# Kernel optimization log

Measured on AMD Instinct MI355X. Metric: run time of the kernel, lower is better.

Reference implementation:

```python
import jax, jax.numpy as jnp
import numpy as np

EPS_LN = 1e-5


def segment_softmax(logits, seg, num_segments):
    m = jax.ops.segment_max(logits, seg, num_segments=num_segments)
    e = jnp.exp(logits - m[seg])
    s = jax.ops.segment_sum(e, seg, num_segments=num_segments)
    return e / (s[seg] + 1e-16)


def transformer_conv(x, src, dst, edge_attr, Wq, bq, Wk, bk, Wv, bv, We, Ws, bs):
    # PyG TransformerConv, heads=1: key/value gathered at source, query at dst,
    # transformed edge feature added to both key and value (message).
    N, D = x.shape[0], Wq.shape[1]
    q = (x @ Wq + bq)[dst]                      # [E, D]
    e = edge_attr @ We                          # [E, D] (lin_edge, no bias)
    k = (x @ Wk + bk)[src] + e                  # [E, D]
    v = (x @ Wv + bv)[src] + e                  # [E, D]
    alpha = segment_softmax((q * k).sum(-1) / jnp.sqrt(jnp.float32(D)), dst, N)
    agg = jax.ops.segment_sum(alpha[:, None] * v, dst, num_segments=N)
    return agg + x @ Ws + bs                    # root_weight skip connection


def graph_layer_norm(x, w, b):
    # PyG LayerNorm mode='graph': normalize over all nodes AND features of the graph.
    mu = x.mean()
    xc = x - mu
    var = (xc * xc).mean()
    return xc * jax.lax.rsqrt(var + EPS_LN) * w + b


def setup_inputs():
    key = jax.random.key(0)
    ks = jax.random.split(key, 32)
    N, E, F_NODE, F_EDGE, H, D_OUT = 50000, 800000, 64, 16, 128, 1
    g = lambda k, shp, s=0.05: jax.random.normal(k, shp, jnp.float32) * s
    inp = {
        'x': jax.random.normal(ks[0], (N, F_NODE), jnp.float32),
        'edge_index': jax.random.randint(ks[1], (2, E), 0, N),
        'edge_attr': jax.random.normal(ks[2], (E, F_EDGE), jnp.float32),
        'fc1_w': g(ks[3], (F_NODE, H)), 'fc1_b': jnp.zeros((H,), jnp.float32),
        'c1_Wq': g(ks[4], (H, H)), 'c1_bq': jnp.zeros((H,), jnp.float32),
        'c1_Wk': g(ks[5], (H, H)), 'c1_bk': jnp.zeros((H,), jnp.float32),
        'c1_Wv': g(ks[6], (H, H)), 'c1_bv': jnp.zeros((H,), jnp.float32),
        'c1_We': g(ks[7], (F_EDGE, H)),
        'c1_Ws': g(ks[8], (H, H)), 'c1_bs': jnp.zeros((H,), jnp.float32),
        'ln1_w': jnp.ones((H,), jnp.float32), 'ln1_b': jnp.zeros((H,), jnp.float32),
        'c2_Wq': g(ks[9], (H, H)), 'c2_bq': jnp.zeros((H,), jnp.float32),
        'c2_Wk': g(ks[10], (H, H)), 'c2_bk': jnp.zeros((H,), jnp.float32),
        'c2_Wv': g(ks[11], (H, H)), 'c2_bv': jnp.zeros((H,), jnp.float32),
        'c2_We': g(ks[12], (F_EDGE, H)),
        'c2_Ws': g(ks[13], (H, H)), 'c2_bs': jnp.zeros((H,), jnp.float32),
        'ln2_w': jnp.ones((H,), jnp.float32), 'ln2_b': jnp.zeros((H,), jnp.float32),
        'fc2_w': g(ks[14], (H, D_OUT)), 'fc2_b': jnp.zeros((D_OUT,), jnp.float32),
    }
    return inp


def reference(x, edge_index, edge_attr,
              fc1_w, fc1_b,
              c1_Wq, c1_bq, c1_Wk, c1_bk, c1_Wv, c1_bv, c1_We, c1_Ws, c1_bs,
              ln1_w, ln1_b,
              c2_Wq, c2_bq, c2_Wk, c2_bk, c2_Wv, c2_bv, c2_We, c2_Ws, c2_bs,
              ln2_w, ln2_b,
              fc2_w, fc2_b):
    src, dst = edge_index[0], edge_index[1]
    hx = x @ fc1_w + fc1_b
    h = transformer_conv(hx, src, dst, edge_attr,
                         c1_Wq, c1_bq, c1_Wk, c1_bk, c1_Wv, c1_bv, c1_We, c1_Ws, c1_bs)
    h = jax.nn.relu(graph_layer_norm(h, ln1_w, ln1_b))
    h = transformer_conv(h, src, dst, edge_attr,
                         c2_Wq, c2_bq, c2_Wk, c2_bk, c2_Wv, c2_bv, c2_We, c2_Ws, c2_bs)
    h = jax.nn.relu(graph_layer_norm(h, ln2_w, ln2_b))
    return h @ fc2_w + fc2_b
```

## Files before the change

### kernel.cpp

```cpp
#include <hip/hip_runtime.h>
#include <math.h>

#define HH 128
#define FIN 64
#define FE 16
#define SCAN_CHUNK 512

__global__ __launch_bounds__(256) void zero_int4(int4* __restrict__ p, int n4) {
  const int stride = gridDim.x * 256;
  for (int i = blockIdx.x * 256 + threadIdx.x; i < n4; i += stride)
    p[i] = make_int4(0, 0, 0, 0);
}

__global__ __launch_bounds__(256) void hist_kernel(
    const int* __restrict__ dstArr, int* __restrict__ deg, int E) {
  const int e = blockIdx.x * 256 + threadIdx.x;
  if (e < E) atomicAdd(deg + dstArr[e], 1);
}

__global__ __launch_bounds__(256) void scan1(
    const int* __restrict__ deg, int* __restrict__ out, int* __restrict__ sums, int n) {
  __shared__ int lds[256];
  const int t = threadIdx.x;
  const int i0 = blockIdx.x * SCAN_CHUNK + t * 2;
  const int v0 = (i0 < n) ? deg[i0] : 0;
  const int v1 = (i0 + 1 < n) ? deg[i0 + 1] : 0;
  const int tsum = v0 + v1;
  lds[t] = tsum;
  __syncthreads();
  for (int off = 1; off < 256; off <<= 1) {
    const int x = (t >= off) ? lds[t - off] : 0;
    __syncthreads();
    lds[t] += x;
    __syncthreads();
  }
  const int excl = lds[t] - tsum;
  if (i0 < n) out[i0] = excl;
  if (i0 + 1 < n) out[i0 + 1] = excl + v0;
  if (t == 255) sums[blockIdx.x] = lds[255];
}

__global__ __launch_bounds__(256) void scan2(int* __restrict__ sums, int nb) {
  __shared__ int lds[256];
  const int t = threadIdx.x;
  const int v = (t < nb) ? sums[t] : 0;
  lds[t] = v;
  __syncthreads();
  for (int off = 1; off < 256; off <<= 1) {
    const int x = (t >= off) ? lds[t - off] : 0;
    __syncthreads();
    lds[t] += x;
    __syncthreads();
  }
  if (t < nb) sums[t] = lds[t] - v;
}

__global__ __launch_bounds__(256) void scan3(
    int* __restrict__ out, const int* __restrict__ sums, int n) {
  const int add = sums[blockIdx.x];
  const int i0 = blockIdx.x * SCAN_CHUNK + threadIdx.x * 2;
  if (i0 < n) out[i0] += add;
  if (i0 + 1 < n) out[i0 + 1] += add;
}

__global__ __launch_bounds__(256) void scatter_kernel(
    const int* __restrict__ dstArr, const int* __restrict__ off,
    int* __restrict__ cursor, int* __restrict__ eids, int E) {
  const int e = blockIdx.x * 256 + threadIdx.x;
  if (e < E) {
    const int d = dstArr[e];
    const int p = atomicAdd(cursor + d, 1);
    eids[off[d] + p] = e;
  }
}

template<int K, int RB>
__global__ __launch_bounds__(128) void gemm_rows(
    const float* __restrict__ in, const float* __restrict__ W,
    const float* __restrict__ bias, float* __restrict__ out, int nrows) {
  __shared__ float tile[RB * K];
  const int r0 = blockIdx.x * RB;
  const int tid = threadIdx.x;
  {
    const int rows = min(RB, nrows - r0);
    const int cnt = rows * K / 4;
    const float4* src = (const float4*)(in + (size_t)r0 * K);
    float4* dst = (float4*)tile;
    for (int i = tid; i < cnt; i += 128) dst[i] = src[i];
  }
  __syncthreads();
  const int j = tid;
  float acc[RB];
  const float bj = bias[j];
#pragma unroll
  for (int r = 0; r < RB; ++r) acc[r] = bj;
#pragma unroll 4
  for (int k = 0; k < K; ++k) {
    float w = W[k * HH + j];
#pragma unroll
    for (int r = 0; r < RB; ++r) acc[r] += tile[r * K + k] * w;
  }
#pragma unroll
  for (int r = 0; r < RB; ++r) {
    int row = r0 + r;
    if (row < nrows) out[(size_t)row * HH + j] = acc[r];
  }
}

template<int RB>
__global__ __launch_bounds__(128) void qkvs_kernel(
    float* __restrict__ x,
    const float* __restrict__ Wq, const float* __restrict__ bq,
    const float* __restrict__ Wk, const float* __restrict__ bk,
    const float* __restrict__ Wv, const float* __restrict__ bv,
    const float* __restrict__ Ws, const float* __restrict__ bs,
    float* __restrict__ q, float* __restrict__ kv,
    int nrows) {
  __shared__ float tile[RB * HH];
  const int r0 = blockIdx.x * RB;
  const int tid = threadIdx.x;
  {
    const int rows = min(RB, nrows - r0);
    const int cnt = rows * HH / 4;
    const float4* src = (const float4*)(x + (size_t)r0 * HH);
    float4* dst = (float4*)tile;
    for (int i = tid; i < cnt; i += 128) dst[i] = src[i];
  }
  __syncthreads();
  const int j = tid;
  float aq[RB], ak[RB], av[RB], as_[RB];
  const float bqj = bq[j], bkj = bk[j], bvj = bv[j], bsj = bs[j];
#pragma unroll
  for (int r = 0; r < RB; ++r) { aq[r] = bqj; ak[r] = bkj; av[r] = bvj; as_[r] = bsj; }
#pragma unroll 2
  for (int kk = 0; kk < HH; ++kk) {
    const float wq = Wq[kk * HH + j];
    const float wk = Wk[kk * HH + j];
    const float wv = Wv[kk * HH + j];
    const float ws = Ws[kk * HH + j];
#pragma unroll
    for (int r = 0; r < RB; ++r) {
      const float xv = tile[r * HH + kk];
      aq[r] += xv * wq; ak[r] += xv * wk; av[r] += xv * wv; as_[r] += xv * ws;
    }
  }
#pragma unroll
  for (int r = 0; r < RB; ++r) {
    int row = r0 + r;
    if (row < nrows) {
      const size_t o = (size_t)row * HH + j;
      const size_t ko = (size_t)row * 256 + j;
      q[o] = aq[r];
      kv[ko] = ak[r];
      kv[ko + HH] = av[r];
      x[o] = as_[r];
    }
  }
}

__global__ __launch_bounds__(128) void qe_kernel(
    const float* __restrict__ q, const float* __restrict__ We,
    float* __restrict__ qe, int N) {
  __shared__ float qs[8 * HH];
  __shared__ float WeT[HH * 17];
  const int tid = threadIdx.x;
  for (int u = tid; u < FE * HH; u += 128) {
    const int i = u >> 7, j = u & 127;
    WeT[j * 17 + i] = We[u];
  }
  const int r0 = blockIdx.x * 8;
  const int rows = min(8, N - r0);
  const int cnt4 = rows * (HH / 4);
  const float4* src = (const float4*)(q + (size_t)r0 * HH);
  for (int u = tid; u < cnt4; u += 128) ((float4*)qs)[u] = src[u];
  __syncthreads();
  const int r = tid >> 4, i = tid & 15;
  if (r < rows) {
    const float* qrow = qs + r * HH;
    float acc = 0.f;
#pragma unroll 8
    for (int j = 0; j < HH; ++j) acc += qrow[j] * WeT[j * 17 + i];
    qe[(size_t)(r0 + r) * FE + i] = acc;
  }
}

__global__ __launch_bounds__(256) void dst_conv16(
    const int* __restrict__ csr_off, const int* __restrict__ deg,
    const int* __restrict__ csr_eid, const int* __restrict__ srcArr,
    const float* __restrict__ ea, const float* __restrict__ We,
    const float* __restrict__ q, const float* __restrict__ qe,
    const float* __restrict__ kv,
    float* __restrict__ xio, double* __restrict__ partials, int N) {
  __shared__ float WeS[FE * HH];
  for (int u = threadIdx.x; u < FE * HH; u += 256) WeS[u] = We[u];
  __syncthreads();
  const int lane = threadIdx.x & 63;
  const int gl = lane & 15;
  const int gbase = lane & 48;
  const int d = (blockIdx.x * 256 + threadIdx.x) >> 4;
  const float rs = 0.088388347648318447f;
  float s = 0.f, sq = 0.f;
  if (d < N) {
    const int off = csr_off[d];
    const int cnt = deg[d];
    const float4* qp = (const float4*)(q + (size_t)d * HH);
    const float4 qc0 = qp[gl], qc1 = qp[16 + gl];
    const float qel = qe[(size_t)d * FE + gl];
    float4 a0 = {0.f, 0.f, 0.f, 0.f}, a1 = {0.f, 0.f, 0.f, 0.f};
    float wsum = 0.f, t = 0.f;
    int i = 0;
    for (; i + 4 <= cnt; i += 4) {
      const int b = off + i;
      const int e0 = csr_eid[b], e1 = csr_eid[b + 1];
      const int e2 = csr_eid[b + 2], e3 = csr_eid[b + 3];
      const int s0 = srcArr[e0], s1 = srcArr[e1];
      const int s2 = srcArr[e2], s3 = srcArr[e3];
      const float A0 = ea[(size_t)e0 * FE + gl];
      const float A1 = ea[(size_t)e1 * FE + gl];
      const float A2 = ea[(size_t)e2 * FE + gl];
      const float A3 = ea[(size_t)e3 * FE + gl];
      const float4* K0 = (const float4*)(kv + (size_t)s0 * 256);
      const float4* K1 = (const float4*)(kv + (size_t)s1 * 256);
      const float4* K2 = (const float4*)(kv + (size_t)s2 * 256);
      const float4* K3 = (const float4*)(kv + (size_t)s3 * 256);
      const float4 k00 = K0[gl], k01 = K0[16 + gl];
      const float4 k10 = K1[gl], k11 = K1[16 + gl];
      const float4 k20 = K2[gl], k21 = K2[16 + gl];
      const float4 k30 = K3[gl], k31 = K3[16 + gl];
      const float4 v00 = K0[32 + gl], v01 = K0[48 + gl];
      const float4 v10 = K1[32 + gl], v11 = K1[48 + gl];
      const float4 v20 = K2[32 + gl], v21 = K2[48 + gl];
      const float4 v30 = K3[32 + gl], v31 = K3[48 + gl];
      float p0 = qc0.x * k00.x + qc0.y * k00.y + qc0.z * k00.z + qc0.w * k00.w
               + qc1.x * k01.x + qc1.y * k01.y + qc1.z * k01.z + qc1.w * k01.w
               + qel * A0;
      float p1 = qc0.x * k10.x + qc0.y * k10.y + qc0.z * k10.z + qc0.w * k10.w
               + qc1.x * k11.x + qc1.y * k11.y + qc1.z * k11.z + qc1.w * k11.w
               + qel * A1;
      float p2 = qc0.x * k20.x + qc0.y * k20.y + qc0.z * k20.z + qc0.w * k20.w
               + qc1.x * k21.x + qc1.y * k21.y + qc1.z * k21.z + qc1.w * k21.w
               + qel * A2;
      float p3 = qc0.x * k30.x + qc0.y * k30.y + qc0.z * k30.z + qc0.w * k30.w
               + qc1.x * k31.x + qc1.y * k31.y + qc1.z * k31.z + qc1.w * k31.w
               + qel * A3;
#pragma unroll
      for (int m = 1; m < 16; m <<= 1) {
        p0 += __shfl_xor(p0, m);
        p1 += __shfl_xor(p1, m);
        p2 += __shfl_xor(p2, m);
        p3 += __shfl_xor(p3, m);
      }
      const float w0 = __expf(p0 * rs);
      const float w1 = __expf(p1 * rs);
      const float w2 = __expf(p2 * rs);
      const float w3 = __expf(p3 * rs);
      a0.x += w0 * v00.x + w1 * v10.x + w2 * v20.x + w3 * v30.x;
      a0.y += w0 * v00.y + w1 * v10.y + w2 * v20.y + w3 * v30.y;
      a0.z += w0 * v00.z + w1 * v10.z + w2 * v20.z + w3 * v30.z;
      a0.w += w0 * v00.w + w1 * v10.w + w2 * v20.w + w3 * v30.w;
      a1.x += w0 * v01.x + w1 * v11.x + w2 * v21.x + w3 * v31.x;
      a1.y += w0 * v01.y + w1 * v11.y + w2 * v21.y + w3 * v31.y;
      a1.z += w0 * v01.z + w1 * v11.z + w2 * v21.z + w3 * v31.z;
      a1.w += w0 * v01.w + w1 * v11.w + w2 * v21.w + w3 * v31.w;
      wsum += (w0 + w1) + (w2 + w3);
      t += w0 * A0 + w1 * A1 + w2 * A2 + w3 * A3;
    }
    for (; i < cnt; ++i) {
      const int e0 = csr_eid[off + i];
      const int s0 = srcArr[e0];
      const float A0 = ea[(size_t)e0 * FE + gl];
      const float4* K0 = (const float4*)(kv + (size_t)s0 * 256);
      const float4 k00 = K0[gl], k01 = K0[16 + gl];
      const float4 v00 = K0[32 + gl], v01 = K0[48 + gl];
      float p0 = qc0.x * k00.x + qc0.y * k00.y + qc0.z * k00.z + qc0.w * k00.w
               + qc1.x * k01.x + qc1.y * k01.y + qc1.z * k01.z + qc1.w * k01.w
               + qel * A0;
#pragma unroll
      for (int m = 1; m < 16; m <<= 1) p0 += __shfl_xor(p0, m);
      const float w0 = __expf(p0 * rs);
      wsum += w0;
      a0.x += w0 * v00.x; a0.y += w0 * v00.y; a0.z += w0 * v00.z; a0.w += w0 * v00.w;
      a1.x += w0 * v01.x; a1.y += w0 * v01.y; a1.z += w0 * v01.z; a1.w += w0 * v01.w;
      t += w0 * A0;
    }
    float4 c0 = {0.f, 0.f, 0.f, 0.f}, c1 = {0.f, 0.f, 0.f, 0.f};
#pragma unroll
    for (int ii = 0; ii < FE; ++ii) {
      const float ti = __shfl(t, gbase + ii);
      const float4 w0 = *(const float4*)(WeS + ii * HH + gl * 4);
      const float4 w1 = *(const float4*)(WeS + ii * HH + 64 + gl * 4);
      c0.x += ti * w0.x; c0.y += ti * w0.y; c0.z += ti * w0.z; c0.w += ti * w0.w;
      c1.x += ti * w1.x; c1.y += ti * w1.y; c1.z += ti * w1.z; c1.w += ti * w1.w;
    }
    const float inv = 1.0f / (wsum + 1e-16f);
    float4* xr = (float4*)(xio + (size_t)d * HH);
    const float4 sk0 = xr[gl], sk1 = xr[16 + gl];
    float4 o0, o1;
    o0.x = fmaf(a0.x + c0.x, inv, sk0.x);
    o0.y = fmaf(a0.y + c0.y, inv, sk0.y);
    o0.z = fmaf(a0.z + c0.z, inv, sk0.z);
    o0.w = fmaf(a0.w + c0.w, inv, sk0.w);
    o1.x = fmaf(a1.x + c1.x, inv, sk1.x);
    o1.y = fmaf(a1.y + c1.y, inv, sk1.y);
    o1.z = fmaf(a1.z + c1.z, inv, sk1.z);
    o1.w = fmaf(a1.w + c1.w, inv, sk1.w);
    xr[gl] = o0;
    xr[16 + gl] = o1;
    s += o0.x + o0.y + o0.z + o0.w + o1.x + o1.y + o1.z + o1.w;
    sq += o0.x * o0.x + o0.y * o0.y + o0.z * o0.z + o0.w * o0.w
        + o1.x * o1.x + o1.y * o1.y + o1.z * o1.z + o1.w * o1.w;
  }
#pragma unroll
  for (int o = 32; o; o >>= 1) {
    s += __shfl_xor(s, o);
    sq += __shfl_xor(sq, o);
  }
  __shared__ double red[8];
  const int w = threadIdx.x >> 6;
  if ((threadIdx.x & 63) == 0) { red[w * 2] = (double)s; red[w * 2 + 1] = (double)sq; }
  __syncthreads();
  if (threadIdx.x == 0) {
    partials[(size_t)blockIdx.x * 2] = red[0] + red[2] + red[4] + red[6];
    partials[(size_t)blockIdx.x * 2 + 1] = red[1] + red[3] + red[5] + red[7];
  }
}

__global__ __launch_bounds__(256) void ln_reduce2(
    const double* __restrict__ partials, int nb, float* __restrict__ stats,
    double inv_count) {
  double s = 0.0, sq = 0.0;
  for (int i = threadIdx.x; i < nb; i += 256) {
    s += partials[(size_t)i * 2];
    sq += partials[(size_t)i * 2 + 1];
  }
#pragma unroll
  for (int off = 32; off; off >>= 1) {
    s += __shfl_xor(s, off);
    sq += __shfl_xor(sq, off);
  }
  __shared__ double red[8];
  const int w = threadIdx.x >> 6;
  if ((threadIdx.x & 63) == 0) { red[w * 2] = s; red[w * 2 + 1] = sq; }
  __syncthreads();
  if (threadIdx.x == 0) {
    double S = 0, SQ = 0;
    for (int i = 0; i < 4; ++i) { S += red[i * 2]; SQ += red[i * 2 + 1]; }
    const double mu = S * inv_count;
    const double var = SQ * inv_count - mu * mu;
    stats[0] = (float)mu;
    stats[1] = (float)(1.0 / sqrt(var + 1e-5));
  }
}

__global__ __launch_bounds__(256) void ln_apply(
    float* __restrict__ x, const float* __restrict__ stats,
    const float* __restrict__ w, const float* __restrict__ b, int total4) {
  const int i = blockIdx.x * 256 + threadIdx.x;
  if (i >= total4) return;
  const float mu = stats[0], rstd = stats[1];
  const float4 xv = ((const float4*)x)[i];
  const float4 wv = ((const float4*)w)[i & 31];
  const float4 bv = ((const float4*)b)[i & 31];
  float4 o;
  o.x = fmaxf(fmaf((xv.x - mu) * rstd, wv.x, bv.x), 0.f);
  o.y = fmaxf(fmaf((xv.y - mu) * rstd, wv.y, bv.y), 0.f);
  o.z = fmaxf(fmaf((xv.z - mu) * rstd, wv.z, bv.z), 0.f);
  o.w = fmaxf(fmaf((xv.w - mu) * rstd, wv.w, bv.w), 0.f);
  ((float4*)x)[i] = o;
}

__global__ __launch_bounds__(256) void fc2_kernel(
    const float* __restrict__ h, const float* __restrict__ w,
    const float* __restrict__ b, float* __restrict__ out, int n) {
  const int lane = threadIdx.x & 63;
  const int node = (blockIdx.x * blockDim.x + threadIdx.x) >> 6;
  if (node >= n) return;
  const float2 hv = *(const float2*)(h + (size_t)node * HH + lane * 2);
  const float2 wv = *(const float2*)(w + lane * 2);
  float p = hv.x * wv.x + hv.y * wv.y;
#pragma unroll
  for (int off = 32; off; off >>= 1) p += __shfl_xor(p, off);
  if (lane == 0) out[node] = p + b[0];
}

extern "C" void kernel_launch(void* const* d_in, const int* in_sizes, int n_in,
                              void* d_out, int out_size, void* d_ws, size_t ws_size,
                              hipStream_t stream) {
  const float* x      = (const float*)d_in[0];
  const int*   eidx   = (const int*)d_in[1];
  const float* ea     = (const float*)d_in[2];
  const float* fc1_w  = (const float*)d_in[3];
  const float* fc1_b  = (const float*)d_in[4];
  const float* c1_Wq  = (const float*)d_in[5];
  const float* c1_bq  = (const float*)d_in[6];
  const float* c1_Wk  = (const float*)d_in[7];
  const float* c1_bk  = (const float*)d_in[8];
  const float* c1_Wv  = (const float*)d_in[9];
  const float* c1_bv  = (const float*)d_in[10];
  const float* c1_We  = (const float*)d_in[11];
  const float* c1_Ws  = (const float*)d_in[12];
  const float* c1_bs  = (const float*)d_in[13];
  const float* ln1_w  = (const float*)d_in[14];
  const float* ln1_b  = (const float*)d_in[15];
  const float* c2_Wq  = (const float*)d_in[16];
  const float* c2_bq  = (const float*)d_in[17];
  const float* c2_Wk  = (const float*)d_in[18];
  const float* c2_bk  = (const float*)d_in[19];
  const float* c2_Wv  = (const float*)d_in[20];
  const float* c2_bv  = (const float*)d_in[21];
  const float* c2_We  = (const float*)d_in[22];
  const float* c2_Ws  = (const float*)d_in[23];
  const float* c2_bs  = (const float*)d_in[24];
  const float* ln2_w  = (const float*)d_in[25];
  const float* ln2_b  = (const float*)d_in[26];
  const float* fc2_w  = (const float*)d_in[27];
  const float* fc2_b  = (const float*)d_in[28];

  const int N = in_sizes[0] / FIN;
  const int E = in_sizes[2] / FE;
  const int* srcA = eidx;
  const int* dstA = eidx + E;

  float* ws    = (float*)d_ws;
  const size_t NH = (size_t)N * HH;
  float* bufX  = ws;
  float* qb    = ws + NH;
  float* kvb   = ws + 2 * NH;
  int* ibase   = (int*)(ws + 4 * NH);
  int* deg     = ibase;
  int* cursor  = ibase + N;
  int* csr_off = ibase + 2 * N;
  int* csr_eid = ibase + 3 * N;
  size_t icnt  = ((size_t)3 * N + E + 3) & ~(size_t)3;
  float* qeb   = (float*)(ibase + icnt);
  double* partials = (double*)(qeb + (size_t)N * FE);
  const int NB = (N * 16 + 255) / 256;
  float* stats = (float*)(partials + 2 * NB);
  int* sums    = (int*)(stats + 4);

  const int total4 = (int)(NH / 4);
  const int gRows  = (N + 15) / 16;
  const int gE     = (E + 255) / 256;
  const int nb1    = (N + SCAN_CHUNK - 1) / SCAN_CHUNK;
  const int gQe    = (N + 7) / 8;
  const double invC = 1.0 / (double)NH;

  zero_int4<<<128, 256, 0, stream>>>((int4*)deg, (2 * N + 3) / 4);
  hist_kernel<<<gE, 256, 0, stream>>>(dstA, deg, E);
  scan1<<<nb1, 256, 0, stream>>>(deg, csr_off, sums, N);
  scan2<<<1, 256, 0, stream>>>(sums, nb1);
  scan3<<<nb1, 256, 0, stream>>>(csr_off, sums, N);
  scatter_kernel<<<gE, 256, 0, stream>>>(dstA, csr_off, cursor, csr_eid, E);

  gemm_rows<FIN, 16><<<gRows, 128, 0, stream>>>(x, fc1_w, fc1_b, bufX, N);
  qkvs_kernel<16><<<gRows, 128, 0, stream>>>(bufX, c1_Wq, c1_bq, c1_Wk, c1_bk,
                                             c1_Wv, c1_bv, c1_Ws, c1_bs,
                                             qb, kvb, N);
  qe_kernel<<<gQe, 128, 0, stream>>>(qb, c1_We, qeb, N);
  dst_conv16<<<NB, 256, 0, stream>>>(csr_off, deg, csr_eid, srcA, ea, c1_We,
                                     qb, qeb, kvb, bufX, partials, N);
  ln_reduce2<<<1, 256, 0, stream>>>(partials, NB, stats, invC);
  ln_apply<<<(total4 + 255) / 256, 256, 0, stream>>>(bufX, stats, ln1_w, ln1_b, total4);

  qkvs_kernel<16><<<gRows, 128, 0, stream>>>(bufX, c2_Wq, c2_bq, c2_Wk, c2_bk,
                                             c2_Wv, c2_bv, c2_Ws, c2_bs,
                                             qb, kvb, N);
  qe_kernel<<<gQe, 128, 0, stream>>>(qb, c2_We, qeb, N);
  dst_conv16<<<NB, 256, 0, stream>>>(csr_off, deg, csr_eid, srcA, ea, c2_We,
                                     qb, qeb, kvb, bufX, partials, N);
  ln_reduce2<<<1, 256, 0, stream>>>(partials, NB, stats, invC);
  ln_apply<<<(total4 + 255) / 256, 256, 0, stream>>>(bufX, stats, ln2_w, ln2_b, total4);

  fc2_kernel<<<(N + 3) / 4, 256, 0, stream>>>(bufX, fc2_w, fc2_b, (float*)d_out, N);
}
```

Baseline: 813.7 us.

## Sort destination nodes by degree for balanced conv waves; vectorize qkvs inner loop

Adds a counting sort of destination nodes by in-degree, in descending order with degrees capped at 255 bins. dst_conv16 then processes nodes through the resulting permutation, so 16-lane groups in the same wavefront handle nodes of similar degree and waste less time on divergent loop trip counts. Separately, the qkvs GEMM inner loop reads four shared-memory x values per float4 load and chains fmaf calls over four k-steps. The sort costs three extra small kernels, and the permuted node order scatters writes to q/xio rows and weakens locality.

Result: slower. 1.067 ms (+31.2%).

```diff
diff --git a/kernel.cpp b/kernel.cpp
--- a/kernel.cpp
+++ b/kernel.cpp
@@ -71,6 +71,39 @@
     const int d = dstArr[e];
     const int p = atomicAdd(cursor + d, 1);
     eids[off[d] + p] = e;
+  }
+}
+
+__global__ __launch_bounds__(256) void hist_deg(
+    const int* __restrict__ deg, int* __restrict__ hist, int N) {
+  const int n = blockIdx.x * 256 + threadIdx.x;
+  if (n < N) atomicAdd(hist + min(deg[n], 255), 1);
+}
+
+__global__ __launch_bounds__(256) void scan_desc(int* __restrict__ hist) {
+  __shared__ int lds[256];
+  const int t = threadIdx.x;
+  const int v = hist[t];
+  lds[t] = v;
+  __syncthreads();
+  for (int off = 1; off < 256; off <<= 1) {
+    const int x = (t >= off) ? lds[t - off] : 0;
+    __syncthreads();
+    lds[t] += x;
+    __syncthreads();
+  }
+  const int total = lds[255];
+  hist[t] = total - lds[t];
+}
+
+__global__ __launch_bounds__(256) void scatter_perm(
+    const int* __restrict__ deg, const int* __restrict__ binoff,
+    int* __restrict__ cursor, int* __restrict__ perm, int N) {
+  const int n = blockIdx.x * 256 + threadIdx.x;
+  if (n < N) {
+    const int b = min(deg[n], 255);
+    const int p = atomicAdd(cursor + b, 1);
+    perm[binoff[b] + p] = n;
   }
 }
 
@@ -133,15 +166,22 @@
 #pragma unroll
   for (int r = 0; r < RB; ++r) { aq[r] = bqj; ak[r] = bkj; av[r] = bvj; as_[r] = bsj; }
 #pragma unroll 2
-  for (int kk = 0; kk < HH; ++kk) {
-    const float wq = Wq[kk * HH + j];
-    const float wk = Wk[kk * HH + j];
-    const float wv = Wv[kk * HH + j];
-    const float ws = Ws[kk * HH + j];
+  for (int kk = 0; kk < HH; kk += 4) {
+    const float wq0 = Wq[(kk + 0) * HH + j], wq1 = Wq[(kk + 1) * HH + j];
+    const float wq2 = Wq[(kk + 2) * HH + j], wq3 = Wq[(kk + 3) * HH + j];
+    const float wk0 = Wk[(kk + 0) * HH + j], wk1 = Wk[(kk + 1) * HH + j];
+    const float wk2 = Wk[(kk + 2) * HH + j], wk3 = Wk[(kk + 3) * HH + j];
+    const float wv0 = Wv[(kk + 0) * HH + j], wv1 = Wv[(kk + 1) * HH + j];
+    const float wv2 = Wv[(kk + 2) * HH + j], wv3 = Wv[(kk + 3) * HH + j];
+    const float ws0 = Ws[(kk + 0) * HH + j], ws1 = Ws[(kk + 1) * HH + j];
+    const float ws2 = Ws[(kk + 2) * HH + j], ws3 = Ws[(kk + 3) * HH + j];
 #pragma unroll
     for (int r = 0; r < RB; ++r) {
-      const float xv = tile[r * HH + kk];
-      aq[r] += xv * wq; ak[r] += xv * wk; av[r] += xv * wv; as_[r] += xv * ws;
+      const float4 xv = *(const float4*)(tile + r * HH + kk);
+      aq[r] = fmaf(xv.x, wq0, fmaf(xv.y, wq1, fmaf(xv.z, wq2, fmaf(xv.w, wq3, aq[r]))));
+      ak[r] = fmaf(xv.x, wk0, fmaf(xv.y, wk1, fmaf(xv.z, wk2, fmaf(xv.w, wk3, ak[r]))));
+      av[r] = fmaf(xv.x, wv0, fmaf(xv.y, wv1, fmaf(xv.z, wv2, fmaf(xv.w, wv3, av[r]))));
+      as_[r] = fmaf(xv.x, ws0, fmaf(xv.y, ws1, fmaf(xv.z, ws2, fmaf(xv.w, ws3, as_[r]))));
     }
   }
 #pragma unroll
@@ -187,6 +227,7 @@
 __global__ __launch_bounds__(256) void dst_conv16(
     const int* __restrict__ csr_off, const int* __restrict__ deg,
     const int* __restrict__ csr_eid, const int* __restrict__ srcArr,
+    const int* __restrict__ perm,
     const float* __restrict__ ea, const float* __restrict__ We,
     const float* __restrict__ q, const float* __restrict__ qe,
     const float* __restrict__ kv,
@@ -197,10 +238,11 @@
   const int lane = threadIdx.x & 63;
   const int gl = lane & 15;
   const int gbase = lane & 48;
-  const int d = (blockIdx.x * 256 + threadIdx.x) >> 4;
+  const int g = (blockIdx.x * 256 + threadIdx.x) >> 4;
   const float rs = 0.088388347648318447f;
   float s = 0.f, sq = 0.f;
-  if (d < N) {
+  if (g < N) {
+    const int d = perm[g];
     const int off = csr_off[d];
     const int cnt = deg[d];
     const float4* qp = (const float4*)(q + (size_t)d * HH);
@@ -429,35 +471,42 @@
   int* ibase   = (int*)(ws + 4 * NH);
   int* deg     = ibase;
   int* cursor  = ibase + N;
-  int* csr_off = ibase + 2 * N;
-  int* csr_eid = ibase + 3 * N;
-  size_t icnt  = ((size_t)3 * N + E + 3) & ~(size_t)3;
+  int* hist2   = ibase + 2 * N;
+  int* cursor2 = ibase + 2 * N + 256;
+  int* csr_off = ibase + 2 * N + 512;
+  int* csr_eid = ibase + 3 * N + 512;
+  int* perm    = ibase + 3 * N + 512 + E;
+  int* sums    = ibase + 4 * N + 512 + E;
+  size_t icnt  = ((size_t)4 * N + 512 + E + 256 + 3) & ~(size_t)3;
   float* qeb   = (float*)(ibase + icnt);
   double* partials = (double*)(qeb + (size_t)N * FE);
   const int NB = (N * 16 + 255) / 256;
   float* stats = (float*)(partials + 2 * NB);
-  int* sums    = (int*)(stats + 4);
 
   const int total4 = (int)(NH / 4);
   const int gRows  = (N + 15) / 16;
   const int gE     = (E + 255) / 256;
+  const int gN     = (N + 255) / 256;
   const int nb1    = (N + SCAN_CHUNK - 1) / SCAN_CHUNK;
   const int gQe    = (N + 7) / 8;
   const double invC = 1.0 / (double)NH;
 
-  zero_int4<<<128, 256, 0, stream>>>((int4*)deg, (2 * N + 3) / 4);
+  zero_int4<<<128, 256, 0, stream>>>((int4*)deg, (2 * N + 512 + 3) / 4);
   hist_kernel<<<gE, 256, 0, stream>>>(dstA, deg, E);
   scan1<<<nb1, 256, 0, stream>>>(deg, csr_off, sums, N);
   scan2<<<1, 256, 0, stream>>>(sums, nb1);
   scan3<<<nb1, 256, 0, stream>>>(csr_off, sums, N);
   scatter_kernel<<<gE, 256, 0, stream>>>(dstA, csr_off, cursor, csr_eid, E);
+  hist_deg<<<gN, 256, 0, stream>>>(deg, hist2, N);
+  scan_desc<<<1, 256, 0, stream>>>(hist2);
+  scatter_perm<<<gN, 256, 0, stream>>>(deg, hist2, cursor2, perm, N);
 
   gemm_rows<FIN, 16><<<gRows, 128, 0, stream>>>(x, fc1_w, fc1_b, bufX, N);
   qkvs_kernel<16><<<gRows, 128, 0, stream>>>(bufX, c1_Wq, c1_bq, c1_Wk, c1_bk,
                                              c1_Wv, c1_bv, c1_Ws, c1_bs,
                                              qb, kvb, N);
   qe_kernel<<<gQe, 128, 0, stream>>>(qb, c1_We, qeb, N);
-  dst_conv16<<<NB, 256, 0, stream>>>(csr_off, deg, csr_eid, srcA, ea, c1_We,
+  dst_conv16<<<NB, 256, 0, stream>>>(csr_off, deg, csr_eid, srcA, perm, ea, c1_We,
                                      qb, qeb, kvb, bufX, partials, N);
   ln_reduce2<<<1, 256, 0, stream>>>(partials, NB, stats, invC);
   ln_apply<<<(total4 + 255) / 256, 256, 0, stream>>>(bufX, stats, ln1_w, ln1_b, total4);
@@ -466,7 +515,7 @@
                                              c2_Wv, c2_bv, c2_Ws, c2_bs,
                                              qb, kvb, N);
   qe_kernel<<<gQe, 128, 0, stream>>>(qb, c2_We, qeb, N);
-  dst_conv16<<<NB, 256, 0, stream>>>(csr_off, deg, csr_eid, srcA, ea, c2_We,
+  dst_conv16<<<NB, 256, 0, stream>>>(csr_off, deg, csr_eid, srcA, perm, ea, c2_We,
                                      qb, qeb, kvb, bufX, partials, N);
   ln_reduce2<<<1, 256, 0, stream>>>(partials, NB, stats, invC);
   ln_apply<<<(total4 + 255) / 256, 256, 0, stream>>>(bufX, stats, ln2_w, ln2_b, total4);
```
